# Optimization experiments

Measured on AMD Instinct MI355X. Metric: run time of the kernel, lower is better.

Reference implementation:

```python
import jax, jax.numpy as jnp
import numpy as np

N_NODES = 50000
N_EDGES = 600000
H = 128


def setup_inputs() -> dict:
    key = jax.random.key(0)
    ks = jax.random.split(key, 6)
    x = jax.random.normal(ks[0], (N_NODES, H), dtype=jnp.float32)
    edge_index = jax.random.randint(ks[1], (2, N_EDGES), 0, N_NODES, dtype=jnp.int64)
    edge_attr = jax.random.normal(ks[2], (N_EDGES, H), dtype=jnp.float32)
    # torch Linear-style params: weight (out, in), bias (out,)
    W1 = jax.random.normal(ks[3], (2 * H, 3 * H), dtype=jnp.float32) * (1.0 / np.sqrt(3 * H))
    b1 = jnp.zeros((2 * H,), dtype=jnp.float32)
    W2 = jax.random.normal(ks[4], (H, 2 * H), dtype=jnp.float32) * (1.0 / np.sqrt(2 * H))
    b2 = jnp.zeros((H,), dtype=jnp.float32)
    return {"x": x, "edge_index": edge_index, "edge_attr": edge_attr,
            "W1": W1, "b1": b1, "W2": W2, "b2": b2}


def reference(x, edge_index, edge_attr, W1, b1, W2, b2):
    row, col = edge_index[0], edge_index[1]
    # gather endpoint features and concat with edge features: [E, 3H]
    out = jnp.concatenate([x[row], x[col], edge_attr], axis=-1)
    h = jax.nn.relu(jnp.einsum('ef,gf->eg', out, W1) + b1)  # [E, 2H]
    return jnp.einsum('eg,hg->eh', h, W2) + b2              # [E, H]
```

## Files before the change

### kernel.cpp

```cpp
#include <hip/hip_runtime.h>
#include <hip/hip_fp16.h>

#define N_NODES 50000
#define N_EDGES 600000

typedef _Float16 f16x8 __attribute__((ext_vector_type(8)));
typedef _Float16 f16x4 __attribute__((ext_vector_type(4)));
typedef float f32x4 __attribute__((ext_vector_type(4)));

#define W1AB_OFF 0
#define W1C_OFF  65536
#define W2_OFF   98304
#define XAB_OFF  131072

__global__ __launch_bounds__(256) void convert_weights(
    const float* __restrict__ W1, const float* __restrict__ W2,
    _Float16* __restrict__ ws16) {
  int i = blockIdx.x * 256 + threadIdx.x;
  if (i < 65536) {
    int n = i >> 7, k = i & 127;
    float v = (n < 256) ? W1[n * 384 + k] : W1[(n - 256) * 384 + 128 + k];
    ws16[W1AB_OFF + i] = (_Float16)v;
  } else if (i < 98304) {
    int j = i - 65536;
    int n = j >> 7, k = j & 127;
    ws16[W1C_OFF + j] = (_Float16)W1[n * 384 + 256 + k];
  } else {
    int j = i - 98304;
    ws16[W2_OFF + j] = (_Float16)W2[j];
  }
}

__global__ __launch_bounds__(256, 2) void node_precompute(
    const float* __restrict__ x, _Float16* __restrict__ ws16) {
  const _Float16* __restrict__ w1ab = ws16 + W1AB_OFF;
  _Float16* __restrict__ xab = ws16 + XAB_OFF;

  __shared__ __align__(16) _Float16 xt[64][136];
  int tid = threadIdx.x;
  int v0 = blockIdx.x * 64;

#pragma unroll
  for (int it = 0; it < 8; ++it) {
    int f = tid + it * 256;
    int r = f >> 5;
    int c = (f & 31) * 4;
    int vr = v0 + r;
    if (vr > N_NODES - 1) vr = N_NODES - 1;
    float4 val = *(const float4*)&x[(size_t)vr * 128 + c];
    f16x4 h;
    h[0] = (_Float16)val.x; h[1] = (_Float16)val.y;
    h[2] = (_Float16)val.z; h[3] = (_Float16)val.w;
    *(f16x4*)&xt[r][c] = h;
  }
  __syncthreads();

  int lane = tid & 63;
  int w = __builtin_amdgcn_readfirstlane(tid >> 6);
  int m16 = lane & 15;
  int quad = lane >> 4;

  for (int nn = 0; nn < 2; ++nn) {
    f32x4 acc[4][4] = {};
#pragma unroll
    for (int kk = 0; kk < 4; ++kk) {
      f16x8 av[4], bv[4];
#pragma unroll
      for (int mb = 0; mb < 4; ++mb)
        av[mb] = *(const f16x8*)&w1ab[(size_t)(w * 128 + nn * 64 + mb * 16 + m16) * 128 +
                                      kk * 32 + quad * 8];
#pragma unroll
      for (int nb = 0; nb < 4; ++nb)
        bv[nb] = *(const f16x8*)&xt[nb * 16 + m16][kk * 32 + quad * 8];
#pragma unroll
      for (int mb = 0; mb < 4; ++mb)
#pragma unroll
        for (int nb = 0; nb < 4; ++nb)
          acc[mb][nb] = __builtin_amdgcn_mfma_f32_16x16x32_f16(av[mb], bv[nb], acc[mb][nb], 0, 0, 0);
    }
#pragma unroll
    for (int mb = 0; mb < 4; ++mb)
#pragma unroll
      for (int nb = 0; nb < 4; ++nb) {
        int v = v0 + nb * 16 + m16;
        if (v < N_NODES) {
          f16x4 hh;
#pragma unroll
          for (int r = 0; r < 4; ++r) hh[r] = (_Float16)acc[mb][nb][r];
          int n = w * 128 + nn * 64 + mb * 16 + quad * 4;
          *(f16x4*)&xab[(size_t)v * 512 + n] = hh;
        }
      }
  }
}

__global__ __launch_bounds__(256, 3) void edge_mlp(
    const int* __restrict__ ei, const float* __restrict__ ea,
    const float* __restrict__ b1, const float* __restrict__ b2,
    const _Float16* __restrict__ ws16, float* __restrict__ out) {
  const _Float16* __restrict__ w1c = ws16 + W1C_OFF;
  const _Float16* __restrict__ w2h = ws16 + W2_OFF;
  const _Float16* __restrict__ xab = ws16 + XAB_OFF;

  __shared__ __align__(16) _Float16 eat[64][136];
  __shared__ __align__(16) _Float16 sh[64][264];

  int tid = threadIdx.x;
  int e0 = blockIdx.x * 64;
  int lane = tid & 63;
  int w = __builtin_amdgcn_readfirstlane(tid >> 6);
  int m16 = lane & 15;
  int quad = lane >> 4;

#pragma unroll
  for (int it = 0; it < 8; ++it) {
    int f = tid + it * 256;
    int r = f >> 5;
    int c = (f & 31) * 4;
    float4 val = *(const float4*)&ea[(size_t)(e0 + r) * 128 + c];
    f16x4 h;
    h[0] = (_Float16)val.x; h[1] = (_Float16)val.y;
    h[2] = (_Float16)val.z; h[3] = (_Float16)val.w;
    *(f16x4*)&eat[r][c] = h;
  }

  int vr[16], vc[16];
#pragma unroll
  for (int i = 0; i < 16; ++i) {
    int a = ei[e0 + w * 16 + i];
    int b = ei[N_EDGES + e0 + w * 16 + i];
    if (a < 0) a = 0;
    if (a > N_NODES - 1) a = N_NODES - 1;
    if (b < 0) b = 0;
    if (b > N_NODES - 1) b = N_NODES - 1;
    vr[i] = a;
    vc[i] = b;
  }

  f16x4 ga[16], gb[16];
#pragma unroll
  for (int i = 0; i < 16; ++i) {
    ga[i] = *(const f16x4*)&xab[(size_t)vr[i] * 512 + lane * 4];
    gb[i] = *(const f16x4*)&xab[(size_t)vc[i] * 512 + 256 + lane * 4];
  }
  f16x4 b1h;
  {
    float4 bb = *(const float4*)&b1[lane * 4];
    b1h[0] = (_Float16)bb.x; b1h[1] = (_Float16)bb.y;
    b1h[2] = (_Float16)bb.z; b1h[3] = (_Float16)bb.w;
  }
#pragma unroll
  for (int i = 0; i < 16; ++i) {
    f16x4 s = ga[i] + gb[i] + b1h;
    *(f16x4*)&sh[w * 16 + i][lane * 4] = s;
  }
  __syncthreads();

  f32x4 acc[4][4] = {};
#pragma unroll
  for (int kk = 0; kk < 4; ++kk) {
    f16x8 av[4], bv[4];
#pragma unroll
    for (int mb = 0; mb < 4; ++mb)
      av[mb] = *(const f16x8*)&w1c[(size_t)(w * 64 + mb * 16 + m16) * 128 + kk * 32 + quad * 8];
#pragma unroll
    for (int eb = 0; eb < 4; ++eb)
      bv[eb] = *(const f16x8*)&eat[eb * 16 + m16][kk * 32 + quad * 8];
#pragma unroll
    for (int mb = 0; mb < 4; ++mb)
#pragma unroll
      for (int eb = 0; eb < 4; ++eb)
        acc[mb][eb] = __builtin_amdgcn_mfma_f32_16x16x32_f16(av[mb], bv[eb], acc[mb][eb], 0, 0, 0);
  }

#pragma unroll
  for (int mb = 0; mb < 4; ++mb)
#pragma unroll
    for (int eb = 0; eb < 4; ++eb) {
      _Float16* p = &sh[eb * 16 + m16][w * 64 + mb * 16 + quad * 4];
      f16x4 s4 = *(const f16x4*)p;
      f16x4 hh;
#pragma unroll
      for (int r = 0; r < 4; ++r) {
        float v = acc[mb][eb][r] + (float)s4[r];
        hh[r] = (_Float16)(v > 0.f ? v : 0.f);
      }
      *(f16x4*)p = hh;
    }
  __syncthreads();

  f32x4 acc2[2][4] = {};
#pragma unroll
  for (int kk = 0; kk < 8; ++kk) {
    f16x8 av[2], bv[4];
#pragma unroll
    for (int mb = 0; mb < 2; ++mb)
      av[mb] = *(const f16x8*)&w2h[(size_t)(w * 32 + mb * 16 + m16) * 256 + kk * 32 + quad * 8];
#pragma unroll
    for (int eb = 0; eb < 4; ++eb)
      bv[eb] = *(const f16x8*)&sh[eb * 16 + m16][kk * 32 + quad * 8];
#pragma unroll
    for (int mb = 0; mb < 2; ++mb)
#pragma unroll
      for (int eb = 0; eb < 4; ++eb)
        acc2[mb][eb] = __builtin_amdgcn_mfma_f32_16x16x32_f16(av[mb], bv[eb], acc2[mb][eb], 0, 0, 0);
  }

  float4 bb2[2];
  bb2[0] = *(const float4*)&b2[w * 32 + quad * 4];
  bb2[1] = *(const float4*)&b2[w * 32 + 16 + quad * 4];
#pragma unroll
  for (int mb = 0; mb < 2; ++mb)
#pragma unroll
    for (int eb = 0; eb < 4; ++eb) {
      float4 o;
      o.x = acc2[mb][eb][0] + bb2[mb].x;
      o.y = acc2[mb][eb][1] + bb2[mb].y;
      o.z = acc2[mb][eb][2] + bb2[mb].z;
      o.w = acc2[mb][eb][3] + bb2[mb].w;
      *(float4*)&out[(size_t)(e0 + eb * 16 + m16) * 128 + w * 32 + mb * 16 + quad * 4] = o;
    }
}

extern "C" void kernel_launch(void* const* d_in, const int* in_sizes, int n_in,
                              void* d_out, int out_size, void* d_ws, size_t ws_size,
                              hipStream_t stream) {
  const float* x  = (const float*)d_in[0];
  const int*   ei = (const int*)d_in[1];
  const float* ea = (const float*)d_in[2];
  const float* W1 = (const float*)d_in[3];
  const float* b1 = (const float*)d_in[4];
  const float* W2 = (const float*)d_in[5];
  const float* b2 = (const float*)d_in[6];
  float* out = (float*)d_out;
  _Float16* ws16 = (_Float16*)d_ws;

  convert_weights<<<512, 256, 0, stream>>>(W1, W2, ws16);
  node_precompute<<<(N_NODES + 63) / 64, 256, 0, stream>>>(x, ws16);
  edge_mlp<<<N_EDGES / 64, 256, 0, stream>>>(ei, ea, b1, b2, ws16, out);
}
```

Before: 680.5 us.

## Load MFMA operands directly from global memory, dropping LDS staging of x and edge_attr

Both node_precompute and edge_mlp now read the x and edge_attr fp32 rows straight into MFMA B-operand registers and convert them to fp16 in place, removing the shared-memory staging tiles. The freed LDS and the raised launch_bounds (4 blocks/SM) aim for higher occupancy. node_precompute also splits its two output halves across blockIdx.y, so x is read twice from global memory. The per-lane loads are less coalesced (two 32-byte reads per row segment), and the barrier in edge_mlp moves after the first GEMM.

After: 898.6 us. 32.0% more time.

```diff
diff --git a/kernel.cpp b/kernel.cpp
--- a/kernel.cpp
+++ b/kernel.cpp
@@ -31,70 +31,64 @@
   }
 }
 
-__global__ __launch_bounds__(256, 2) void node_precompute(
+__global__ __launch_bounds__(256, 4) void node_precompute(
     const float* __restrict__ x, _Float16* __restrict__ ws16) {
   const _Float16* __restrict__ w1ab = ws16 + W1AB_OFF;
   _Float16* __restrict__ xab = ws16 + XAB_OFF;
 
-  __shared__ __align__(16) _Float16 xt[64][136];
   int tid = threadIdx.x;
   int v0 = blockIdx.x * 64;
-
-#pragma unroll
-  for (int it = 0; it < 8; ++it) {
-    int f = tid + it * 256;
-    int r = f >> 5;
-    int c = (f & 31) * 4;
-    int vr = v0 + r;
-    if (vr > N_NODES - 1) vr = N_NODES - 1;
-    float4 val = *(const float4*)&x[(size_t)vr * 128 + c];
-    f16x4 h;
-    h[0] = (_Float16)val.x; h[1] = (_Float16)val.y;
-    h[2] = (_Float16)val.z; h[3] = (_Float16)val.w;
-    *(f16x4*)&xt[r][c] = h;
-  }
-  __syncthreads();
-
+  int nn = blockIdx.y;
   int lane = tid & 63;
   int w = __builtin_amdgcn_readfirstlane(tid >> 6);
   int m16 = lane & 15;
   int quad = lane >> 4;
 
-  for (int nn = 0; nn < 2; ++nn) {
-    f32x4 acc[4][4] = {};
-#pragma unroll
-    for (int kk = 0; kk < 4; ++kk) {
-      f16x8 av[4], bv[4];
-#pragma unroll
-      for (int mb = 0; mb < 4; ++mb)
-        av[mb] = *(const f16x8*)&w1ab[(size_t)(w * 128 + nn * 64 + mb * 16 + m16) * 128 +
-                                      kk * 32 + quad * 8];
+  f32x4 acc[4][4] = {};
+#pragma unroll
+  for (int kk = 0; kk < 4; ++kk) {
+    f16x8 bv[4];
+#pragma unroll
+    for (int nb = 0; nb < 4; ++nb) {
+      int v = v0 + nb * 16 + m16;
+      if (v > N_NODES - 1) v = N_NODES - 1;
+      const float* p = &x[(size_t)v * 128 + kk * 32 + quad * 8];
+      float4 p0 = *(const float4*)p;
+      float4 p1 = *(const float4*)(p + 4);
+      f16x8 b;
+      b[0] = (_Float16)p0.x; b[1] = (_Float16)p0.y;
+      b[2] = (_Float16)p0.z; b[3] = (_Float16)p0.w;
+      b[4] = (_Float16)p1.x; b[5] = (_Float16)p1.y;
+      b[6] = (_Float16)p1.z; b[7] = (_Float16)p1.w;
+      bv[nb] = b;
+    }
+    f16x8 av[4];
+#pragma unroll
+    for (int mb = 0; mb < 4; ++mb)
+      av[mb] = *(const f16x8*)&w1ab[(size_t)(w * 128 + nn * 64 + mb * 16 + m16) * 128 +
+                                    kk * 32 + quad * 8];
+#pragma unroll
+    for (int mb = 0; mb < 4; ++mb)
 #pragma unroll
       for (int nb = 0; nb < 4; ++nb)
-        bv[nb] = *(const f16x8*)&xt[nb * 16 + m16][kk * 32 + quad * 8];
-#pragma unroll
-      for (int mb = 0; mb < 4; ++mb)
-#pragma unroll
-        for (int nb = 0; nb < 4; ++nb)
-          acc[mb][nb] = __builtin_amdgcn_mfma_f32_16x16x32_f16(av[mb], bv[nb], acc[mb][nb], 0, 0, 0);
-    }
-#pragma unroll
-    for (int mb = 0; mb < 4; ++mb)
-#pragma unroll
-      for (int nb = 0; nb < 4; ++nb) {
-        int v = v0 + nb * 16 + m16;
-        if (v < N_NODES) {
-          f16x4 hh;
-#pragma unroll
-          for (int r = 0; r < 4; ++r) hh[r] = (_Float16)acc[mb][nb][r];
-          int n = w * 128 + nn * 64 + mb * 16 + quad * 4;
-          *(f16x4*)&xab[(size_t)v * 512 + n] = hh;
-        }
+        acc[mb][nb] = __builtin_amdgcn_mfma_f32_16x16x32_f16(av[mb], bv[nb], acc[mb][nb], 0, 0, 0);
+  }
+#pragma unroll
+  for (int mb = 0; mb < 4; ++mb)
+#pragma unroll
+    for (int nb = 0; nb < 4; ++nb) {
+      int v = v0 + nb * 16 + m16;
+      if (v < N_NODES) {
+        f16x4 hh;
+#pragma unroll
+        for (int r = 0; r < 4; ++r) hh[r] = (_Float16)acc[mb][nb][r];
+        int n = w * 128 + nn * 64 + mb * 16 + quad * 4;
+        *(f16x4*)&xab[(size_t)v * 512 + n] = hh;
       }
-  }
-}
-
-__global__ __launch_bounds__(256, 3) void edge_mlp(
+    }
+}
+
+__global__ __launch_bounds__(256, 4) void edge_mlp(
     const int* __restrict__ ei, const float* __restrict__ ea,
     const float* __restrict__ b1, const float* __restrict__ b2,
     const _Float16* __restrict__ ws16, float* __restrict__ out) {
@@ -102,7 +96,6 @@
   const _Float16* __restrict__ w2h = ws16 + W2_OFF;
   const _Float16* __restrict__ xab = ws16 + XAB_OFF;
 
-  __shared__ __align__(16) _Float16 eat[64][136];
   __shared__ __align__(16) _Float16 sh[64][264];
 
   int tid = threadIdx.x;
@@ -111,18 +104,6 @@
   int w = __builtin_amdgcn_readfirstlane(tid >> 6);
   int m16 = lane & 15;
   int quad = lane >> 4;
-
-#pragma unroll
-  for (int it = 0; it < 8; ++it) {
-    int f = tid + it * 256;
-    int r = f >> 5;
-    int c = (f & 31) * 4;
-    float4 val = *(const float4*)&ea[(size_t)(e0 + r) * 128 + c];
-    f16x4 h;
-    h[0] = (_Float16)val.x; h[1] = (_Float16)val.y;
-    h[2] = (_Float16)val.z; h[3] = (_Float16)val.w;
-    *(f16x4*)&eat[r][c] = h;
-  }
 
   int vr[16], vc[16];
 #pragma unroll
@@ -154,7 +135,6 @@
     f16x4 s = ga[i] + gb[i] + b1h;
     *(f16x4*)&sh[w * 16 + i][lane * 4] = s;
   }
-  __syncthreads();
 
   f32x4 acc[4][4] = {};
 #pragma unroll
@@ -164,14 +144,24 @@
     for (int mb = 0; mb < 4; ++mb)
       av[mb] = *(const f16x8*)&w1c[(size_t)(w * 64 + mb * 16 + m16) * 128 + kk * 32 + quad * 8];
 #pragma unroll
-    for (int eb = 0; eb < 4; ++eb)
-      bv[eb] = *(const f16x8*)&eat[eb * 16 + m16][kk * 32 + quad * 8];
+    for (int eb = 0; eb < 4; ++eb) {
+      const float* p = &ea[(size_t)(e0 + eb * 16 + m16) * 128 + kk * 32 + quad * 8];
+      float4 p0 = *(const float4*)p;
+      float4 p1 = *(const float4*)(p + 4);
+      f16x8 b;
+      b[0] = (_Float16)p0.x; b[1] = (_Float16)p0.y;
+      b[2] = (_Float16)p0.z; b[3] = (_Float16)p0.w;
+      b[4] = (_Float16)p1.x; b[5] = (_Float16)p1.y;
+      b[6] = (_Float16)p1.z; b[7] = (_Float16)p1.w;
+      bv[eb] = b;
+    }
 #pragma unroll
     for (int mb = 0; mb < 4; ++mb)
 #pragma unroll
       for (int eb = 0; eb < 4; ++eb)
         acc[mb][eb] = __builtin_amdgcn_mfma_f32_16x16x32_f16(av[mb], bv[eb], acc[mb][eb], 0, 0, 0);
   }
+  __syncthreads();
 
 #pragma unroll
   for (int mb = 0; mb < 4; ++mb)
@@ -236,6 +226,6 @@
   _Float16* ws16 = (_Float16*)d_ws;
 
   convert_weights<<<512, 256, 0, stream>>>(W1, W2, ws16);
-  node_precompute<<<(N_NODES + 63) / 64, 256, 0, stream>>>(x, ws16);
+  node_precompute<<<dim3((N_NODES + 63) / 64, 2), 256, 0, stream>>>(x, ws16);
   edge_mlp<<<N_EDGES / 64, 256, 0, stream>>>(ei, ea, b1, b2, ws16, out);
 }
```
